# Kernel optimization log

Measured on AMD Instinct MI355X. Metric: run time of the kernel, lower is better.

Reference implementation:

```python
import jax, jax.numpy as jnp
import numpy as np

N = 100000   # nodes
B = 64       # graphs in batch
E = 1600000  # edges
D_IN = 2
W1D = W2D = W3D = 128
N_CLASSES = 3
MIN_SCORE = 0.1
TOL = 1e-7
BN_EPS = 1e-5


def setup_inputs() -> dict:
    key = jax.random.key(0)
    ks = jax.random.split(key, 32)
    inp = {}
    inp['x'] = jax.random.normal(ks[0], (N, D_IN), jnp.float32)
    inp['edge_index'] = jax.random.randint(ks[1], (2, E), 0, N, dtype=jnp.int32)
    inp['batch_index'] = jnp.sort(jax.random.randint(ks[2], (N,), 0, B, dtype=jnp.int32))
    inp['topk_w'] = jax.random.normal(ks[3], (D_IN,), jnp.float32)
    dims = [(D_IN, W1D), (W1D, W2D), (W2D, W3D)]
    k = 4
    for i, (din, dout) in enumerate(dims, start=1):
        inp[f'W{i}'] = jax.random.normal(ks[k], (din, dout), jnp.float32) * (1.0 / np.sqrt(din)); k += 1
        inp[f'b{i}'] = jax.random.normal(ks[k], (dout,), jnp.float32) * 0.05; k += 1
        inp[f'g{i}'] = 1.0 + 0.1 * jax.random.normal(ks[k], (dout,), jnp.float32); k += 1
        inp[f'be{i}'] = 0.1 * jax.random.normal(ks[k], (dout,), jnp.float32); k += 1
        inp[f'rm{i}'] = 0.1 * jax.random.normal(ks[k], (dout,), jnp.float32); k += 1
        inp[f'rv{i}'] = 1.0 + 0.1 * jax.random.uniform(ks[k], (dout,), jnp.float32); k += 1
    inp['linW'] = jax.random.normal(ks[k], (W3D, N_CLASSES), jnp.float32) * (1.0 / np.sqrt(W3D)); k += 1
    inp['linb'] = jax.random.normal(ks[k], (N_CLASSES,), jnp.float32) * 0.05
    return inp


def _bn_eval(x, g, be, rm, rv):
    # BatchNorm1d in eval mode (running stats)
    return (x - rm) * jax.lax.rsqrt(rv + BN_EPS) * g + be


def _gcn(x, src, dst, ew, W, b):
    # GCNConv: lin -> symmetric-normalized scatter-add (self-loops already in src/dst/ew)
    xw = x @ W                                   # [N, dout]
    deg = jax.ops.segment_sum(ew, dst, num_segments=N)
    dinv = jnp.where(deg > 0, jax.lax.rsqrt(deg), 0.0)
    norm = dinv[src] * ew * dinv[dst]            # [E+N]
    out = jax.ops.segment_sum(norm[:, None] * xw[src], dst, num_segments=N)
    return out + b


def reference(x, edge_index, batch_index, topk_w,
              W1, b1, g1, be1, rm1, rv1,
              W2, b2, g2, be2, rm2, rv2,
              W3, b3, g3, be3, rm3, rv3,
              linW, linb):
    # ---- TopKPooling (min_score mode): per-graph softmax score, threshold keep,
    # x scaled by score. Implemented via masking (fixed shapes): dropped nodes get
    # zero features, zero edge weights, and -inf at the max pool -> math identical
    # to PyG's node filtering (BN is eval-mode, i.e. per-node).
    logits = x @ topk_w                                                    # [N]
    m = jax.ops.segment_max(logits, batch_index, num_segments=B)
    e = jnp.exp(logits - m[batch_index])
    score = e / jax.ops.segment_sum(e, batch_index, num_segments=B)[batch_index]
    smax = jax.ops.segment_max(score, batch_index, num_segments=B)[batch_index] - TOL
    keep = score > jnp.minimum(smax, MIN_SCORE)                            # [N] bool
    keep_f = keep.astype(x.dtype)
    h = x * (score * keep_f)[:, None]

    src0, dst0 = edge_index[0], edge_index[1]
    loop = jnp.arange(N, dtype=src0.dtype)
    src = jnp.concatenate([src0, loop])
    dst = jnp.concatenate([dst0, loop])
    ew = jnp.concatenate([keep_f[src0] * keep_f[dst0], keep_f])            # mask + self-loops

    h = _bn_eval(jax.nn.relu(_gcn(h, src, dst, ew, W1, b1)), g1, be1, rm1, rv1)
    h = _bn_eval(jax.nn.relu(_gcn(h, src, dst, ew, W2, b2)), g2, be2, rm2, rv2)
    h = _bn_eval(jax.nn.relu(_gcn(h, src, dst, ew, W3, b3)), g3, be3, rm3, rv3)

    neg = jnp.finfo(h.dtype).min
    h = jnp.where(keep[:, None], h, neg)
    pooled = jax.ops.segment_max(h, batch_index, num_segments=B)           # [B, w3]
    out = pooled @ linW + linb
    return jax.nn.log_softmax(out, axis=1)
```

## Files before the change

### kernel.cpp

```cpp
#include <hip/hip_runtime.h>

#define NN 100000
#define BB 64
#define EE 1600000
#define FD 128
#define SLOTC 64
#define KSLOTS (BB * SLOTC)
#define EMAXE (1 << 20)
#define NWORDS (NN / 32)
#define STR 391

__device__ __forceinline__ int plower(const int* __restrict__ bidx, int v,
                                      int tid, int* ired) {
    int p = tid * STR;
    int val = bidx[p];
    ired[tid] = (val < v) ? tid : -1;
    __syncthreads();
    for (int s = 128; s > 0; s >>= 1) { if (tid < s) ired[tid] = max(ired[tid], ired[tid + s]); __syncthreads(); }
    int t0 = ired[0];
    __syncthreads();
    if (t0 < 0) return 0;
    int lo = t0 * STR;
    int hi = lo + STR; if (hi > NN) hi = NN;
    int ans = hi;
    for (int q = lo + 1 + tid; q < hi; q += 256) {
        if (bidx[q] >= v) { ans = q; break; }
    }
    ired[tid] = ans;
    __syncthreads();
    for (int s = 128; s > 0; s >>= 1) { if (tid < s) ired[tid] = min(ired[tid], ired[tid + s]); __syncthreads(); }
    int r = ired[0];
    __syncthreads();
    return r;
}

__global__ __launch_bounds__(256) void k_scorekeep(
    const float2* __restrict__ x, const int* __restrict__ bidx,
    const float* __restrict__ tw,
    unsigned* __restrict__ kfbits, int* __restrict__ nslot,
    int* __restrict__ knt, float* __restrict__ degs, float2* __restrict__ h0s,
    int* __restrict__ kecnt)
{
    __shared__ int   ired[256];
    __shared__ float red[256];
    __shared__ int   klist[SLOTC];
    __shared__ int   lcnt;
    __shared__ float shv;
    int b = blockIdx.x, tid = threadIdx.x;
    if (tid == 0) { lcnt = 0; if (b == 0) { kecnt[0] = 0; kecnt[1] = 0; } }
    int s0 = plower(bidx, b, tid, ired);
    int e0 = plower(bidx, b + 1, tid, ired);
    int L = e0 - s0;
    float w0 = tw[0], w1 = tw[1];

    if (L > 0) {
        int wlo = s0 >> 5, whi = (e0 - 1) >> 5;
        for (int w = wlo + tid; w <= whi; w += 256) {
            unsigned mask = 0xFFFFFFFFu;
            if (w == wlo) mask &= (0xFFFFFFFFu << (s0 & 31));
            if (w == whi) mask &= (0xFFFFFFFFu >> (31 - ((e0 - 1) & 31)));
            if (mask == 0xFFFFFFFFu) kfbits[w] = 0u;
            else atomicAnd(&kfbits[w], ~mask);
        }
    }

    float mx = -3.4028235e38f;
    for (int j = tid; j < L; j += 256) {
        float2 v = x[s0 + j];
        mx = fmaxf(mx, v.x * w0 + v.y * w1);
    }
    red[tid] = mx; __syncthreads();
    for (int s = 128; s > 0; s >>= 1) { if (tid < s) red[tid] = fmaxf(red[tid], red[tid + s]); __syncthreads(); }
    if (tid == 0) shv = red[0];
    __syncthreads();
    float m = shv;

    float sm = 0.f;
    for (int j = tid; j < L; j += 256) {
        float2 v = x[s0 + j];
        sm += expf(v.x * w0 + v.y * w1 - m);
    }
    red[tid] = sm; __syncthreads();
    for (int s = 128; s > 0; s >>= 1) { if (tid < s) red[tid] += red[tid + s]; __syncthreads(); }
    if (tid == 0) shv = red[0];
    __syncthreads();
    float S = shv;
    float thr = fminf(1.0f / S - 1e-7f, 0.1f);

    for (int j = tid; j < L; j += 256) {
        float2 v = x[s0 + j];
        float sc = expf(v.x * w0 + v.y * w1 - m) / S;
        if (sc > thr) {
            int l = atomicAdd(&lcnt, 1);
            if (l < SLOTC) klist[l] = j;
        }
    }
    __syncthreads();
    int nk = lcnt; if (nk > SLOTC) nk = SLOTC;
    if (tid == 0) knt[b] = nk;
    for (int l = tid; l < nk; l += 256) {
        int i = s0 + klist[l];
        float2 v = x[i];
        float sc = expf(v.x * w0 + v.y * w1 - m) / S;
        int slot = b * SLOTC + l;
        atomicOr(&kfbits[i >> 5], 1u << (i & 31));
        nslot[i] = slot;
        degs[slot] = 1.0f;
        h0s[slot] = make_float2(v.x * sc, v.y * sc);
    }
}

__global__ void k_edges(const int4* __restrict__ src4, const int* __restrict__ ei,
                        const unsigned* __restrict__ kfbits, const int* __restrict__ nslot,
                        float* __restrict__ degs, int* __restrict__ kedge,
                        int* __restrict__ kecnt) {
    int t = blockIdx.x * 256 + threadIdx.x;
    if (t * 4 >= EE) return;
    int4 s4 = src4[t];
    int ss[4] = {s4.x, s4.y, s4.z, s4.w};
    #pragma unroll
    for (int q = 0; q < 4; q++) {
        int s = ss[q];
        if ((kfbits[s >> 5] >> (s & 31)) & 1u) {
            int d = ei[EE + t * 4 + q];
            if ((kfbits[d >> 5] >> (d & 31)) & 1u) {
                int ds = nslot[d], sl = nslot[s];
                atomicAdd(&degs[ds], 1.0f);
                int idx = atomicAdd(&kecnt[0], 1);
                if (idx < EMAXE) { kedge[2 * idx] = sl; kedge[2 * idx + 1] = ds; }
                if ((sl >> 6) != (ds >> 6)) atomicAdd(&kecnt[1], 1);
            }
        }
    }
}

__global__ __launch_bounds__(256) void k_tail_main(
    const float* __restrict__ degs, const float2* __restrict__ h0s,
    const int* __restrict__ kedge, const int* __restrict__ kecnt,
    const int* __restrict__ knt,
    const float* __restrict__ W1, const float* __restrict__ b1,
    const float* __restrict__ g1, const float* __restrict__ be1,
    const float* __restrict__ rm1, const float* __restrict__ rv1,
    const float* __restrict__ W2, const float* __restrict__ b2,
    const float* __restrict__ g2, const float* __restrict__ be2,
    const float* __restrict__ rm2, const float* __restrict__ rv2,
    const float* __restrict__ W3, const float* __restrict__ b3,
    const float* __restrict__ g3, const float* __restrict__ be3,
    const float* __restrict__ rm3, const float* __restrict__ rv3,
    const float* __restrict__ linW, const float* __restrict__ linb,
    float* __restrict__ hY, float* __restrict__ out)
{
    __shared__ float tileA[SLOTC * FD];
    __shared__ float tileB[SLOTC * FD];
    __shared__ float2 psl[SLOTC];
    __shared__ float poolv[FD];
    __shared__ int keS;
    int b = blockIdx.x, tid = threadIdx.x;
    if (tid == 0) { int k = kecnt[0]; keS = k > EMAXE ? EMAXE : k; }
    for (int j = tid; j < SLOTC; j += 256) psl[j] = make_float2(0.f, 0.f);
    __syncthreads();
    int ke = keS, nk = knt[b], cross = kecnt[1];

    for (int t = tid; t < ke; t += 256) {
        int d = kedge[2 * t + 1];
        if ((d >> 6) == b) {
            int s = kedge[2 * t];
            float nm = rsqrtf(degs[s]) * rsqrtf(degs[d]);
            float2 h = h0s[s];
            atomicAdd(&psl[d & 63].x, nm * h.x);
            atomicAdd(&psl[d & 63].y, nm * h.y);
        }
    }
    __syncthreads();
    for (int j = tid; j < nk * FD; j += 256) {
        int ld = j >> 7, f = j & 127, slot = b * SLOTC + ld;
        float di = rsqrtf(degs[slot]), d2 = di * di;
        float2 h = h0s[slot];
        float a0 = psl[ld].x + d2 * h.x;
        float a1 = psl[ld].y + d2 * h.y;
        float v = a0 * W1[f] + a1 * W1[FD + f] + b1[f];
        v = fmaxf(v, 0.f);
        v = (v - rm1[f]) * rsqrtf(rv1[f] + 1e-5f) * g1[f] + be1[f];
        tileA[j] = v;
    }
    __syncthreads();
    for (int j = tid; j < nk * FD; j += 256) {
        int ld = j >> 7, f = j & 127;
        const float* xr = tileA + ld * FD;
        float acc = 0.f;
        #pragma unroll 8
        for (int k = 0; k < FD; k++) acc += xr[k] * W2[k * FD + f];
        tileB[j] = acc;
    }
    __syncthreads();
    if (cross != 0) {
        for (int j = tid; j < nk * FD; j += 256) {
            int ld = j >> 7, f = j & 127;
            hY[(b * SLOTC + ld) * FD + f] = tileB[j];
        }
        return;
    }
    for (int j = tid; j < nk * FD; j += 256) tileA[j] = 0.f;
    __syncthreads();
    for (long long idx = tid; idx < (long long)ke * FD; idx += 256) {
        int e = (int)(idx >> 7), f = (int)(idx & 127);
        int d = kedge[2 * e + 1];
        if ((d >> 6) == b) {
            int s = kedge[2 * e];
            float nm = rsqrtf(degs[s]) * rsqrtf(degs[d]);
            atomicAdd(&tileA[(d & 63) * FD + f], nm * tileB[(s & 63) * FD + f]);
        }
    }
    __syncthreads();
    for (int j = tid; j < nk * FD; j += 256) {
        int ld = j >> 7, f = j & 127, slot = b * SLOTC + ld;
        float di = rsqrtf(degs[slot]);
        float v = tileA[j] + di * di * tileB[j] + b2[f];
        v = fmaxf(v, 0.f);
        v = (v - rm2[f]) * rsqrtf(rv2[f] + 1e-5f) * g2[f] + be2[f];
        tileA[j] = v;
    }
    __syncthreads();
    for (int j = tid; j < nk * FD; j += 256) {
        int ld = j >> 7, f = j & 127;
        const float* xr = tileA + ld * FD;
        float acc = 0.f;
        #pragma unroll 8
        for (int k = 0; k < FD; k++) acc += xr[k] * W3[k * FD + f];
        tileB[j] = acc;
    }
    __syncthreads();
    for (int j = tid; j < nk * FD; j += 256) tileA[j] = 0.f;
    __syncthreads();
    for (long long idx = tid; idx < (long long)ke * FD; idx += 256) {
        int e = (int)(idx >> 7), f = (int)(idx & 127);
        int d = kedge[2 * e + 1];
        if ((d >> 6) == b) {
            int s = kedge[2 * e];
            float nm = rsqrtf(degs[s]) * rsqrtf(degs[d]);
            atomicAdd(&tileA[(d & 63) * FD + f], nm * tileB[(s & 63) * FD + f]);
        }
    }
    __syncthreads();
    for (int j = tid; j < nk * FD; j += 256) {
        int ld = j >> 7, f = j & 127, slot = b * SLOTC + ld;
        float di = rsqrtf(degs[slot]);
        float v = tileA[j] + di * di * tileB[j] + b3[f];
        v = fmaxf(v, 0.f);
        v = (v - rm3[f]) * rsqrtf(rv3[f] + 1e-5f) * g3[f] + be3[f];
        tileA[j] = v;
    }
    __syncthreads();
    for (int f = tid; f < FD; f += 256) {
        float mx = -3.4028235e38f;
        for (int ld = 0; ld < nk; ld++) mx = fmaxf(mx, tileA[ld * FD + f]);
        poolv[f] = mx;
    }
    __syncthreads();
    if (tid == 0) {
        float z0 = linb[0], z1 = linb[1], z2 = linb[2];
        for (int f = 0; f < FD; f++) {
            float pv = poolv[f];
            z0 += pv * linW[f * 3 + 0];
            z1 += pv * linW[f * 3 + 1];
            z2 += pv * linW[f * 3 + 2];
        }
        float m = fmaxf(z0, fmaxf(z1, z2));
        float l = m + logf(expf(z0 - m) + expf(z1 - m) + expf(z2 - m));
        out[b * 3 + 0] = z0 - l;
        out[b * 3 + 1] = z1 - l;
        out[b * 3 + 2] = z2 - l;
    }
}

__global__ __launch_bounds__(256) void k_tail_slow(
    const float* __restrict__ degs, const int* __restrict__ kedge,
    const int* __restrict__ kecnt, const int* __restrict__ knt,
    const float* __restrict__ hY,
    const float* __restrict__ b2, const float* __restrict__ g2,
    const float* __restrict__ be2, const float* __restrict__ rm2,
    const float* __restrict__ rv2,
    const float* __restrict__ W3, const float* __restrict__ b3,
    const float* __restrict__ g3, const float* __restrict__ be3,
    const float* __restrict__ rm3, const float* __restrict__ rv3,
    const float* __restrict__ linW, const float* __restrict__ linb,
    float* __restrict__ out)
{
    if (kecnt[1] == 0) return;
    __shared__ float tileA[SLOTC * FD];
    __shared__ float tileB[SLOTC * FD];
    __shared__ float rowt[FD];
    __shared__ float poolv[FD];
    __shared__ int keS;
    int b = blockIdx.x, tid = threadIdx.x;
    if (tid == 0) { int k = kecnt[0]; keS = k > EMAXE ? EMAXE : k; }
    __syncthreads();
    int ke = keS, nk = knt[b];

    for (int j = tid; j < nk * FD; j += 256) tileA[j] = 0.f;
    __syncthreads();
    for (long long idx = tid; idx < (long long)ke * FD; idx += 256) {
        int e = (int)(idx >> 7), f = (int)(idx & 127);
        int d = kedge[2 * e + 1];
        if ((d >> 6) == b) {
            int s = kedge[2 * e];
            float nm = rsqrtf(degs[s]) * rsqrtf(degs[d]);
            atomicAdd(&tileA[(d & 63) * FD + f], nm * hY[s * FD + f]);
        }
    }
    __syncthreads();
    for (int j = tid; j < nk * FD; j += 256) {
        int ld = j >> 7, f = j & 127, slot = b * SLOTC + ld;
        float di = rsqrtf(degs[slot]);
        float v = tileA[j] + di * di * hY[slot * FD + f] + b2[f];
        v = fmaxf(v, 0.f);
        v = (v - rm2[f]) * rsqrtf(rv2[f] + 1e-5f) * g2[f] + be2[f];
        tileA[j] = v;
    }
    __syncthreads();
    for (int j = tid; j < nk * FD; j += 256) {
        int ld = j >> 7, f = j & 127;
        const float* xr = tileA + ld * FD;
        float acc = 0.f;
        #pragma unroll 8
        for (int k = 0; k < FD; k++) acc += xr[k] * W3[k * FD + f];
        tileB[j] = acc;
    }
    __syncthreads();
    for (int j = tid; j < nk * FD; j += 256) tileA[j] = 0.f;
    __syncthreads();
    for (long long idx = tid; idx < (long long)ke * FD; idx += 256) {
        int e = (int)(idx >> 7), f = (int)(idx & 127);
        int d = kedge[2 * e + 1];
        if ((d >> 6) == b) {
            int s = kedge[2 * e];
            if ((s >> 6) == b) {
                float nm = rsqrtf(degs[s]) * rsqrtf(degs[d]);
                atomicAdd(&tileA[(d & 63) * FD + f], nm * tileB[(s & 63) * FD + f]);
            }
        }
    }
    __syncthreads();
    for (int e = 0; e < ke; e++) {
        int d = kedge[2 * e + 1];
        if ((d >> 6) != b) continue;
        int s = kedge[2 * e];
        if ((s >> 6) == b) continue;
        float dis = rsqrtf(degs[s]);
        for (int f = tid; f < FD; f += 256) {
            float acc = dis * dis * hY[s * FD + f];
            for (int e2 = 0; e2 < ke; e2++) {
                if (kedge[2 * e2 + 1] == s) {
                    int u = kedge[2 * e2];
                    acc += rsqrtf(degs[u]) * dis * hY[u * FD + f];
                }
            }
            float v = acc + b2[f];
            v = fmaxf(v, 0.f);
            v = (v - rm2[f]) * rsqrtf(rv2[f] + 1e-5f) * g2[f] + be2[f];
            rowt[f] = v;
        }
        __syncthreads();
        float nm = dis * rsqrtf(degs[d]);
        for (int f = tid; f < FD; f += 256) {
            float acc = 0.f;
            #pragma unroll 8
            for (int k = 0; k < FD; k++) acc += rowt[k] * W3[k * FD + f];
            atomicAdd(&tileA[(d & 63) * FD + f], nm * acc);
        }
        __syncthreads();
    }
    for (int j = tid; j < nk * FD; j += 256) {
        int ld = j >> 7, f = j & 127, slot = b * SLOTC + ld;
        float di = rsqrtf(degs[slot]);
        float v = tileA[j] + di * di * tileB[j] + b3[f];
        v = fmaxf(v, 0.f);
        v = (v - rm3[f]) * rsqrtf(rv3[f] + 1e-5f) * g3[f] + be3[f];
        tileA[j] = v;
    }
    __syncthreads();
    for (int f = tid; f < FD; f += 256) {
        float mx = -3.4028235e38f;
        for (int ld = 0; ld < nk; ld++) mx = fmaxf(mx, tileA[ld * FD + f]);
        poolv[f] = mx;
    }
    __syncthreads();
    if (tid == 0) {
        float z0 = linb[0], z1 = linb[1], z2 = linb[2];
        for (int f = 0; f < FD; f++) {
            float pv = poolv[f];
            z0 += pv * linW[f * 3 + 0];
            z1 += pv * linW[f * 3 + 1];
            z2 += pv * linW[f * 3 + 2];
        }
        float m = fmaxf(z0, fmaxf(z1, z2));
        float l = m + logf(expf(z0 - m) + expf(z1 - m) + expf(z2 - m));
        out[b * 3 + 0] = z0 - l;
        out[b * 3 + 1] = z1 - l;
        out[b * 3 + 2] = z2 - l;
    }
}

extern "C" void kernel_launch(void* const* d_in, const int* in_sizes, int n_in,
                              void* d_out, int out_size, void* d_ws, size_t ws_size,
                              hipStream_t stream) {
    (void)in_sizes; (void)n_in; (void)out_size; (void)ws_size;
    const float* x    = (const float*)d_in[0];
    const int*   ei   = (const int*)d_in[1];
    const int*   bidx = (const int*)d_in[2];
    const float* tw   = (const float*)d_in[3];
    const float* W1 = (const float*)d_in[4],  *b1 = (const float*)d_in[5],  *g1 = (const float*)d_in[6];
    const float* be1= (const float*)d_in[7],  *rm1= (const float*)d_in[8],  *rv1= (const float*)d_in[9];
    const float* W2 = (const float*)d_in[10], *b2 = (const float*)d_in[11], *g2 = (const float*)d_in[12];
    const float* be2= (const float*)d_in[13], *rm2= (const float*)d_in[14], *rv2= (const float*)d_in[15];
    const float* W3 = (const float*)d_in[16], *b3 = (const float*)d_in[17], *g3 = (const float*)d_in[18];
    const float* be3= (const float*)d_in[19], *rm3= (const float*)d_in[20], *rv3= (const float*)d_in[21];
    const float* linW = (const float*)d_in[22], *linb = (const float*)d_in[23];
    float* out = (float*)d_out;

    char* w = (char*)d_ws;
    auto take = [&](size_t bytes) { char* r = w; w += (bytes + 255) & ~(size_t)255; return r; };
    int*      kecnt  = (int*)take(16);
    int*      knt    = (int*)take((size_t)BB * 4);
    unsigned* kfbits = (unsigned*)take((size_t)NWORDS * 4);
    int*      nslot  = (int*)take((size_t)NN * 4);
    float*    degs   = (float*)take((size_t)KSLOTS * 4);
    float2*   h0s    = (float2*)take((size_t)KSLOTS * 8);
    int*      kedge  = (int*)take((size_t)EMAXE * 8);
    float*    hY     = (float*)take((size_t)KSLOTS * FD * 4);

    k_scorekeep<<<BB, 256, 0, stream>>>((const float2*)x, bidx, tw,
                                        kfbits, nslot, knt, degs, h0s, kecnt);
    k_edges<<<(EE / 4 + 255) / 256, 256, 0, stream>>>((const int4*)ei, ei, kfbits,
                                                      nslot, degs, kedge, kecnt);
    k_tail_main<<<BB, 256, 0, stream>>>(degs, h0s, kedge, kecnt, knt,
                                        W1, b1, g1, be1, rm1, rv1,
                                        W2, b2, g2, be2, rm2, rv2,
                                        W3, b3, g3, be3, rm3, rv3,
                                        linW, linb, hY, out);
    k_tail_slow<<<BB, 256, 0, stream>>>(degs, kedge, kecnt, knt, hY,
                                        b2, g2, be2, rm2, rv2,
                                        W3, b3, g3, be3, rm3, rv3,
                                        linW, linb, out);
}
```

Baseline: 143.2 us.

## Fuse score, edge filter and GCN tail into one cooperative kernel

Merges the four kernel launches into a single cooperative kernel of 256 blocks that uses grid-wide syncs between the scoring, edge-filtering and tail phases. The edge phase becomes a grid-stride loop over all edges. The aim is to remove per-launch overhead and inter-kernel gaps, and it keeps the old multi-kernel path as a fallback if the cooperative launch fails. In exchange, the edge scan runs on far fewer blocks than the previous 1563, the shared-memory footprint per block grows because score and tail storage are combined, and grid syncs add their own cost.

```diff
diff --git a/kernel.cpp b/kernel.cpp
--- a/kernel.cpp
+++ b/kernel.cpp
@@ -1,4 +1,7 @@
 #include <hip/hip_runtime.h>
+#include <hip/hip_cooperative_groups.h>
+
+namespace cg = cooperative_groups;
 
 #define NN 100000
 #define BB 64
@@ -9,6 +12,21 @@
 #define EMAXE (1 << 20)
 #define NWORDS (NN / 32)
 #define STR 391
+#define GRID_F 256
+
+struct KArgs {
+    const float2* x; const int4* src4; const int* ei; const int* bidx; const float* tw;
+    const float *W1,*b1,*g1,*be1,*rm1,*rv1;
+    const float *W2,*b2,*g2,*be2,*rm2,*rv2;
+    const float *W3,*b3,*g3,*be3,*rm3,*rv3;
+    const float *linW,*linb;
+    unsigned* kfbits; int* nslot; int* knt; float* degs; float2* h0s;
+    int* kedge; int* kecnt; float* hY; float* out;
+};
+
+struct LdsScore { int ired[256]; float red[256]; int klist[SLOTC]; int lcnt; float shv; };
+struct LdsTail  { float tileA[SLOTC*FD]; float tileB[SLOTC*FD]; float2 psl[SLOTC];
+                  float poolv[FD]; float rowt[FD]; };
 
 __device__ __forceinline__ int plower(const int* __restrict__ bidx, int v,
                                       int tid, int* ired) {
@@ -34,371 +52,356 @@
     return r;
 }
 
-__global__ __launch_bounds__(256) void k_scorekeep(
-    const float2* __restrict__ x, const int* __restrict__ bidx,
-    const float* __restrict__ tw,
-    unsigned* __restrict__ kfbits, int* __restrict__ nslot,
-    int* __restrict__ knt, float* __restrict__ degs, float2* __restrict__ h0s,
-    int* __restrict__ kecnt)
-{
-    __shared__ int   ired[256];
-    __shared__ float red[256];
-    __shared__ int   klist[SLOTC];
-    __shared__ int   lcnt;
-    __shared__ float shv;
-    int b = blockIdx.x, tid = threadIdx.x;
-    if (tid == 0) { lcnt = 0; if (b == 0) { kecnt[0] = 0; kecnt[1] = 0; } }
-    int s0 = plower(bidx, b, tid, ired);
-    int e0 = plower(bidx, b + 1, tid, ired);
-    int L = e0 - s0;
-    float w0 = tw[0], w1 = tw[1];
-
-    if (L > 0) {
+__device__ void phase_score(const KArgs& a, int b, int tid, LdsScore& L) {
+    if (tid == 0) { L.lcnt = 0; if (b == 0) { a.kecnt[0] = 0; a.kecnt[1] = 0; } }
+    int s0 = plower(a.bidx, b, tid, L.ired);
+    int e0 = plower(a.bidx, b + 1, tid, L.ired);
+    int Ln = e0 - s0;
+    float w0 = a.tw[0], w1 = a.tw[1];
+
+    if (Ln > 0) {
         int wlo = s0 >> 5, whi = (e0 - 1) >> 5;
         for (int w = wlo + tid; w <= whi; w += 256) {
             unsigned mask = 0xFFFFFFFFu;
             if (w == wlo) mask &= (0xFFFFFFFFu << (s0 & 31));
             if (w == whi) mask &= (0xFFFFFFFFu >> (31 - ((e0 - 1) & 31)));
-            if (mask == 0xFFFFFFFFu) kfbits[w] = 0u;
-            else atomicAnd(&kfbits[w], ~mask);
+            if (mask == 0xFFFFFFFFu) a.kfbits[w] = 0u;
+            else atomicAnd(&a.kfbits[w], ~mask);
         }
     }
 
     float mx = -3.4028235e38f;
-    for (int j = tid; j < L; j += 256) {
-        float2 v = x[s0 + j];
+    for (int j = tid; j < Ln; j += 256) {
+        float2 v = a.x[s0 + j];
         mx = fmaxf(mx, v.x * w0 + v.y * w1);
     }
-    red[tid] = mx; __syncthreads();
-    for (int s = 128; s > 0; s >>= 1) { if (tid < s) red[tid] = fmaxf(red[tid], red[tid + s]); __syncthreads(); }
-    if (tid == 0) shv = red[0];
-    __syncthreads();
-    float m = shv;
+    L.red[tid] = mx; __syncthreads();
+    for (int s = 128; s > 0; s >>= 1) { if (tid < s) L.red[tid] = fmaxf(L.red[tid], L.red[tid + s]); __syncthreads(); }
+    if (tid == 0) L.shv = L.red[0];
+    __syncthreads();
+    float m = L.shv;
 
     float sm = 0.f;
-    for (int j = tid; j < L; j += 256) {
-        float2 v = x[s0 + j];
+    for (int j = tid; j < Ln; j += 256) {
+        float2 v = a.x[s0 + j];
         sm += expf(v.x * w0 + v.y * w1 - m);
     }
-    red[tid] = sm; __syncthreads();
-    for (int s = 128; s > 0; s >>= 1) { if (tid < s) red[tid] += red[tid + s]; __syncthreads(); }
-    if (tid == 0) shv = red[0];
-    __syncthreads();
-    float S = shv;
+    L.red[tid] = sm; __syncthreads();
+    for (int s = 128; s > 0; s >>= 1) { if (tid < s) L.red[tid] += L.red[tid + s]; __syncthreads(); }
+    if (tid == 0) L.shv = L.red[0];
+    __syncthreads();
+    float S = L.shv;
     float thr = fminf(1.0f / S - 1e-7f, 0.1f);
 
-    for (int j = tid; j < L; j += 256) {
-        float2 v = x[s0 + j];
+    for (int j = tid; j < Ln; j += 256) {
+        float2 v = a.x[s0 + j];
         float sc = expf(v.x * w0 + v.y * w1 - m) / S;
         if (sc > thr) {
-            int l = atomicAdd(&lcnt, 1);
-            if (l < SLOTC) klist[l] = j;
-        }
-    }
-    __syncthreads();
-    int nk = lcnt; if (nk > SLOTC) nk = SLOTC;
-    if (tid == 0) knt[b] = nk;
+            int l = atomicAdd(&L.lcnt, 1);
+            if (l < SLOTC) L.klist[l] = j;
+        }
+    }
+    __syncthreads();
+    int nk = L.lcnt; if (nk > SLOTC) nk = SLOTC;
+    if (tid == 0) a.knt[b] = nk;
     for (int l = tid; l < nk; l += 256) {
-        int i = s0 + klist[l];
-        float2 v = x[i];
+        int i = s0 + L.klist[l];
+        float2 v = a.x[i];
         float sc = expf(v.x * w0 + v.y * w1 - m) / S;
         int slot = b * SLOTC + l;
-        atomicOr(&kfbits[i >> 5], 1u << (i & 31));
-        nslot[i] = slot;
-        degs[slot] = 1.0f;
-        h0s[slot] = make_float2(v.x * sc, v.y * sc);
-    }
-}
-
-__global__ void k_edges(const int4* __restrict__ src4, const int* __restrict__ ei,
-                        const unsigned* __restrict__ kfbits, const int* __restrict__ nslot,
-                        float* __restrict__ degs, int* __restrict__ kedge,
-                        int* __restrict__ kecnt) {
-    int t = blockIdx.x * 256 + threadIdx.x;
-    if (t * 4 >= EE) return;
-    int4 s4 = src4[t];
-    int ss[4] = {s4.x, s4.y, s4.z, s4.w};
-    #pragma unroll
-    for (int q = 0; q < 4; q++) {
-        int s = ss[q];
-        if ((kfbits[s >> 5] >> (s & 31)) & 1u) {
-            int d = ei[EE + t * 4 + q];
-            if ((kfbits[d >> 5] >> (d & 31)) & 1u) {
-                int ds = nslot[d], sl = nslot[s];
-                atomicAdd(&degs[ds], 1.0f);
-                int idx = atomicAdd(&kecnt[0], 1);
-                if (idx < EMAXE) { kedge[2 * idx] = sl; kedge[2 * idx + 1] = ds; }
-                if ((sl >> 6) != (ds >> 6)) atomicAdd(&kecnt[1], 1);
+        atomicOr(&a.kfbits[i >> 5], 1u << (i & 31));
+        a.nslot[i] = slot;
+        a.degs[slot] = 1.0f;
+        a.h0s[slot] = make_float2(v.x * sc, v.y * sc);
+    }
+}
+
+__device__ void phase_edges(const KArgs& a, int t0, int stride) {
+    const int M = EE / 4;
+    for (int t = t0; t < M; t += stride) {
+        int4 s4 = a.src4[t];
+        int ss[4] = {s4.x, s4.y, s4.z, s4.w};
+        #pragma unroll
+        for (int q = 0; q < 4; q++) {
+            int s = ss[q];
+            if ((a.kfbits[s >> 5] >> (s & 31)) & 1u) {
+                int d = a.ei[EE + t * 4 + q];
+                if ((a.kfbits[d >> 5] >> (d & 31)) & 1u) {
+                    int ds = a.nslot[d], sl = a.nslot[s];
+                    atomicAdd(&a.degs[ds], 1.0f);
+                    int idx = atomicAdd(&a.kecnt[0], 1);
+                    if (idx < EMAXE) { a.kedge[2 * idx] = sl; a.kedge[2 * idx + 1] = ds; }
+                    if ((sl >> 6) != (ds >> 6)) atomicAdd(&a.kecnt[1], 1);
+                }
             }
         }
     }
 }
 
-__global__ __launch_bounds__(256) void k_tail_main(
-    const float* __restrict__ degs, const float2* __restrict__ h0s,
-    const int* __restrict__ kedge, const int* __restrict__ kecnt,
-    const int* __restrict__ knt,
-    const float* __restrict__ W1, const float* __restrict__ b1,
-    const float* __restrict__ g1, const float* __restrict__ be1,
-    const float* __restrict__ rm1, const float* __restrict__ rv1,
-    const float* __restrict__ W2, const float* __restrict__ b2,
-    const float* __restrict__ g2, const float* __restrict__ be2,
-    const float* __restrict__ rm2, const float* __restrict__ rv2,
-    const float* __restrict__ W3, const float* __restrict__ b3,
-    const float* __restrict__ g3, const float* __restrict__ be3,
-    const float* __restrict__ rm3, const float* __restrict__ rv3,
-    const float* __restrict__ linW, const float* __restrict__ linb,
-    float* __restrict__ hY, float* __restrict__ out)
-{
-    __shared__ float tileA[SLOTC * FD];
-    __shared__ float tileB[SLOTC * FD];
-    __shared__ float2 psl[SLOTC];
-    __shared__ float poolv[FD];
-    __shared__ int keS;
-    int b = blockIdx.x, tid = threadIdx.x;
-    if (tid == 0) { int k = kecnt[0]; keS = k > EMAXE ? EMAXE : k; }
-    for (int j = tid; j < SLOTC; j += 256) psl[j] = make_float2(0.f, 0.f);
-    __syncthreads();
-    int ke = keS, nk = knt[b], cross = kecnt[1];
-
+__device__ void tail_common(const KArgs& a, int b, int tid, LdsTail& T, int ke, int nk) {
+    for (int j = tid; j < SLOTC; j += 256) T.psl[j] = make_float2(0.f, 0.f);
+    __syncthreads();
     for (int t = tid; t < ke; t += 256) {
-        int d = kedge[2 * t + 1];
+        int d = a.kedge[2 * t + 1];
         if ((d >> 6) == b) {
-            int s = kedge[2 * t];
-            float nm = rsqrtf(degs[s]) * rsqrtf(degs[d]);
-            float2 h = h0s[s];
-            atomicAdd(&psl[d & 63].x, nm * h.x);
-            atomicAdd(&psl[d & 63].y, nm * h.y);
+            int s = a.kedge[2 * t];
+            float nm = rsqrtf(a.degs[s]) * rsqrtf(a.degs[d]);
+            float2 h = a.h0s[s];
+            atomicAdd(&T.psl[d & 63].x, nm * h.x);
+            atomicAdd(&T.psl[d & 63].y, nm * h.y);
         }
     }
     __syncthreads();
     for (int j = tid; j < nk * FD; j += 256) {
         int ld = j >> 7, f = j & 127, slot = b * SLOTC + ld;
-        float di = rsqrtf(degs[slot]), d2 = di * di;
-        float2 h = h0s[slot];
-        float a0 = psl[ld].x + d2 * h.x;
-        float a1 = psl[ld].y + d2 * h.y;
-        float v = a0 * W1[f] + a1 * W1[FD + f] + b1[f];
+        float di = rsqrtf(a.degs[slot]), d2 = di * di;
+        float2 h = a.h0s[slot];
+        float a0 = T.psl[ld].x + d2 * h.x;
+        float a1 = T.psl[ld].y + d2 * h.y;
+        float v = a0 * a.W1[f] + a1 * a.W1[FD + f] + a.b1[f];
         v = fmaxf(v, 0.f);
-        v = (v - rm1[f]) * rsqrtf(rv1[f] + 1e-5f) * g1[f] + be1[f];
-        tileA[j] = v;
+        v = (v - a.rm1[f]) * rsqrtf(a.rv1[f] + 1e-5f) * a.g1[f] + a.be1[f];
+        T.tileA[j] = v;
     }
     __syncthreads();
     for (int j = tid; j < nk * FD; j += 256) {
         int ld = j >> 7, f = j & 127;
-        const float* xr = tileA + ld * FD;
+        const float* xr = T.tileA + ld * FD;
         float acc = 0.f;
         #pragma unroll 8
-        for (int k = 0; k < FD; k++) acc += xr[k] * W2[k * FD + f];
-        tileB[j] = acc;
-    }
-    __syncthreads();
-    if (cross != 0) {
-        for (int j = tid; j < nk * FD; j += 256) {
-            int ld = j >> 7, f = j & 127;
-            hY[(b * SLOTC + ld) * FD + f] = tileB[j];
-        }
-        return;
-    }
-    for (int j = tid; j < nk * FD; j += 256) tileA[j] = 0.f;
+        for (int k = 0; k < FD; k++) acc += xr[k] * a.W2[k * FD + f];
+        T.tileB[j] = acc;
+    }
+    __syncthreads();
+}
+
+__device__ void tail_write_hY(const KArgs& a, int b, int tid, LdsTail& T, int nk) {
+    for (int j = tid; j < nk * FD; j += 256) {
+        int ld = j >> 7, f = j & 127;
+        a.hY[(b * SLOTC + ld) * FD + f] = T.tileB[j];
+    }
+}
+
+__device__ void tail_out(const KArgs& a, int b, int tid, LdsTail& T, int nk) {
+    for (int f = tid; f < FD; f += 256) {
+        float mx = -3.4028235e38f;
+        for (int ld = 0; ld < nk; ld++) mx = fmaxf(mx, T.tileA[ld * FD + f]);
+        T.poolv[f] = mx;
+    }
+    __syncthreads();
+    if (tid == 0) {
+        float z0 = a.linb[0], z1 = a.linb[1], z2 = a.linb[2];
+        for (int f = 0; f < FD; f++) {
+            float pv = T.poolv[f];
+            z0 += pv * a.linW[f * 3 + 0];
+            z1 += pv * a.linW[f * 3 + 1];
+            z2 += pv * a.linW[f * 3 + 2];
+        }
+        float m = fmaxf(z0, fmaxf(z1, z2));
+        float l = m + logf(expf(z0 - m) + expf(z1 - m) + expf(z2 - m));
+        a.out[b * 3 + 0] = z0 - l;
+        a.out[b * 3 + 1] = z1 - l;
+        a.out[b * 3 + 2] = z2 - l;
+    }
+}
+
+__device__ void tail_fast(const KArgs& a, int b, int tid, LdsTail& T, int ke, int nk) {
+    for (int j = tid; j < nk * FD; j += 256) T.tileA[j] = 0.f;
     __syncthreads();
     for (long long idx = tid; idx < (long long)ke * FD; idx += 256) {
         int e = (int)(idx >> 7), f = (int)(idx & 127);
-        int d = kedge[2 * e + 1];
+        int d = a.kedge[2 * e + 1];
         if ((d >> 6) == b) {
-            int s = kedge[2 * e];
-            float nm = rsqrtf(degs[s]) * rsqrtf(degs[d]);
-            atomicAdd(&tileA[(d & 63) * FD + f], nm * tileB[(s & 63) * FD + f]);
+            int s = a.kedge[2 * e];
+            float nm = rsqrtf(a.degs[s]) * rsqrtf(a.degs[d]);
+            atomicAdd(&T.tileA[(d & 63) * FD + f], nm * T.tileB[(s & 63) * FD + f]);
         }
     }
     __syncthreads();
     for (int j = tid; j < nk * FD; j += 256) {
         int ld = j >> 7, f = j & 127, slot = b * SLOTC + ld;
-        float di = rsqrtf(degs[slot]);
-        float v = tileA[j] + di * di * tileB[j] + b2[f];
+        float di = rsqrtf(a.degs[slot]);
+        float v = T.tileA[j] + di * di * T.tileB[j] + a.b2[f];
         v = fmaxf(v, 0.f);
-        v = (v - rm2[f]) * rsqrtf(rv2[f] + 1e-5f) * g2[f] + be2[f];
-        tileA[j] = v;
+        v = (v - a.rm2[f]) * rsqrtf(a.rv2[f] + 1e-5f) * a.g2[f] + a.be2[f];
+        T.tileA[j] = v;
     }
     __syncthreads();
     for (int j = tid; j < nk * FD; j += 256) {
         int ld = j >> 7, f = j & 127;
-        const float* xr = tileA + ld * FD;
+        const float* xr = T.tileA + ld * FD;
         float acc = 0.f;
         #pragma unroll 8
-        for (int k = 0; k < FD; k++) acc += xr[k] * W3[k * FD + f];
-        tileB[j] = acc;
-    }
-    __syncthreads();
-    for (int j = tid; j < nk * FD; j += 256) tileA[j] = 0.f;
+        for (int k = 0; k < FD; k++) acc += xr[k] * a.W3[k * FD + f];
+        T.tileB[j] = acc;
+    }
+    __syncthreads();
+    for (int j = tid; j < nk * FD; j += 256) T.tileA[j] = 0.f;
     __syncthreads();
     for (long long idx = tid; idx < (long long)ke * FD; idx += 256) {
         int e = (int)(idx >> 7), f = (int)(idx & 127);
-        int d = kedge[2 * e + 1];
+        int d = a.kedge[2 * e + 1];
         if ((d >> 6) == b) {
-            int s = kedge[2 * e];
-            float nm = rsqrtf(degs[s]) * rsqrtf(degs[d]);
-            atomicAdd(&tileA[(d & 63) * FD + f], nm * tileB[(s & 63) * FD + f]);
+            int s = a.kedge[2 * e];
+            float nm = rsqrtf(a.degs[s]) * rsqrtf(a.degs[d]);
+            atomicAdd(&T.tileA[(d & 63) * FD + f], nm * T.tileB[(s & 63) * FD + f]);
         }
     }
     __syncthreads();
     for (int j = tid; j < nk * FD; j += 256) {
         int ld = j >> 7, f = j & 127, slot = b * SLOTC + ld;
-        float di = rsqrtf(degs[slot]);
-        float v = tileA[j] + di * di * tileB[j] + b3[f];
+        float di = rsqrtf(a.degs[slot]);
+        float v = T.tileA[j] + di * di * T.tileB[j] + a.b3[f];
         v = fmaxf(v, 0.f);
-        v = (v - rm3[f]) * rsqrtf(rv3[f] + 1e-5f) * g3[f] + be3[f];
-        tileA[j] = v;
-    }
-    __syncthreads();
-    for (int f = tid; f < FD; f += 256) {
-        float mx = -3.4028235e38f;
-        for (int ld = 0; ld < nk; ld++) mx = fmaxf(mx, tileA[ld * FD + f]);
-        poolv[f] = mx;
-    }
-    __syncthreads();
-    if (tid == 0) {
-        float z0 = linb[0], z1 = linb[1], z2 = linb[2];
-        for (int f = 0; f < FD; f++) {
-            float pv = poolv[f];
-            z0 += pv * linW[f * 3 + 0];
-            z1 += pv * linW[f * 3 + 1];
-            z2 += pv * linW[f * 3 + 2];
-        }
-        float m = fmaxf(z0, fmaxf(z1, z2));
-        float l = m + logf(expf(z0 - m) + expf(z1 - m) + expf(z2 - m));
-        out[b * 3 + 0] = z0 - l;
-        out[b * 3 + 1] = z1 - l;
-        out[b * 3 + 2] = z2 - l;
-    }
-}
-
-__global__ __launch_bounds__(256) void k_tail_slow(
-    const float* __restrict__ degs, const int* __restrict__ kedge,
-    const int* __restrict__ kecnt, const int* __restrict__ knt,
-    const float* __restrict__ hY,
-    const float* __restrict__ b2, const float* __restrict__ g2,
-    const float* __restrict__ be2, const float* __restrict__ rm2,
-    const float* __restrict__ rv2,
-    const float* __restrict__ W3, const float* __restrict__ b3,
-    const float* __restrict__ g3, const float* __restrict__ be3,
-    const float* __restrict__ rm3, const float* __restrict__ rv3,
-    const float* __restrict__ linW, const float* __restrict__ linb,
-    float* __restrict__ out)
-{
-    if (kecnt[1] == 0) return;
-    __shared__ float tileA[SLOTC * FD];
-    __shared__ float tileB[SLOTC * FD];
-    __shared__ float rowt[FD];
-    __shared__ float poolv[FD];
-    __shared__ int keS;
-    int b = blockIdx.x, tid = threadIdx.x;
-    if (tid == 0) { int k = kecnt[0]; keS = k > EMAXE ? EMAXE : k; }
-    __syncthreads();
-    int ke = keS, nk = knt[b];
-
-    for (int j = tid; j < nk * FD; j += 256) tileA[j] = 0.f;
+        v = (v - a.rm3[f]) * rsqrtf(a.rv3[f] + 1e-5f) * a.g3[f] + a.be3[f];
+        T.tileA[j] = v;
+    }
+    __syncthreads();
+    tail_out(a, b, tid, T, nk);
+}
+
+__device__ void tail_slow(const KArgs& a, int b, int tid, LdsTail& T, int ke, int nk) {
+    for (int j = tid; j < nk * FD; j += 256) T.tileA[j] = 0.f;
     __syncthreads();
     for (long long idx = tid; idx < (long long)ke * FD; idx += 256) {
         int e = (int)(idx >> 7), f = (int)(idx & 127);
-        int d = kedge[2 * e + 1];
+        int d = a.kedge[2 * e + 1];
         if ((d >> 6) == b) {
-            int s = kedge[2 * e];
-            float nm = rsqrtf(degs[s]) * rsqrtf(degs[d]);
-            atomicAdd(&tileA[(d & 63) * FD + f], nm * hY[s * FD + f]);
+            int s = a.kedge[2 * e];
+            float nm = rsqrtf(a.degs[s]) * rsqrtf(a.degs[d]);
+            atomicAdd(&T.tileA[(d & 63) * FD + f], nm * a.hY[s * FD + f]);
         }
     }
     __syncthreads();
     for (int j = tid; j < nk * FD; j += 256) {
         int ld = j >> 7, f = j & 127, slot = b * SLOTC + ld;
-        float di = rsqrtf(degs[slot]);
-        float v = tileA[j] + di * di * hY[slot * FD + f] + b2[f];
+        float di = rsqrtf(a.degs[slot]);
+        float v = T.tileA[j] + di * di * a.hY[slot * FD + f] + a.b2[f];
         v = fmaxf(v, 0.f);
-        v = (v - rm2[f]) * rsqrtf(rv2[f] + 1e-5f) * g2[f] + be2[f];
-        tileA[j] = v;
+        v = (v - a.rm2[f]) * rsqrtf(a.rv2[f] + 1e-5f) * a.g2[f] + a.be2[f];
+        T.tileA[j] = v;
     }
     __syncthreads();
     for (int j = tid; j < nk * FD; j += 256) {
         int ld = j >> 7, f = j & 127;
-        const float* xr = tileA + ld * FD;
+        const float* xr = T.tileA + ld * FD;
         float acc = 0.f;
         #pragma unroll 8
-        for (int k = 0; k < FD; k++) acc += xr[k] * W3[k * FD + f];
-        tileB[j] = acc;
-    }
-    __syncthreads();
-    for (int j = tid; j < nk * FD; j += 256) tileA[j] = 0.f;
+        for (int k = 0; k < FD; k++) acc += xr[k] * a.W3[k * FD + f];
+        T.tileB[j] = acc;
+    }
+    __syncthreads();
+    for (int j = tid; j < nk * FD; j += 256) T.tileA[j] = 0.f;
     __syncthreads();
     for (long long idx = tid; idx < (long long)ke * FD; idx += 256) {
         int e = (int)(idx >> 7), f = (int)(idx & 127);
-        int d = kedge[2 * e + 1];
+        int d = a.kedge[2 * e + 1];
         if ((d >> 6) == b) {
-            int s = kedge[2 * e];
+            int s = a.kedge[2 * e];
             if ((s >> 6) == b) {
-                float nm = rsqrtf(degs[s]) * rsqrtf(degs[d]);
-                atomicAdd(&tileA[(d & 63) * FD + f], nm * tileB[(s & 63) * FD + f]);
+                float nm = rsqrtf(a.degs[s]) * rsqrtf(a.degs[d]);
+                atomicAdd(&T.tileA[(d & 63) * FD + f], nm * T.tileB[(s & 63) * FD + f]);
             }
         }
     }
     __syncthreads();
     for (int e = 0; e < ke; e++) {
-        int d = kedge[2 * e + 1];
+        int d = a.kedge[2 * e + 1];
         if ((d >> 6) != b) continue;
-        int s = kedge[2 * e];
+        int s = a.kedge[2 * e];
         if ((s >> 6) == b) continue;
-        float dis = rsqrtf(degs[s]);
+        float dis = rsqrtf(a.degs[s]);
         for (int f = tid; f < FD; f += 256) {
-            float acc = dis * dis * hY[s * FD + f];
+            float acc = dis * dis * a.hY[s * FD + f];
             for (int e2 = 0; e2 < ke; e2++) {
-                if (kedge[2 * e2 + 1] == s) {
-                    int u = kedge[2 * e2];
-                    acc += rsqrtf(degs[u]) * dis * hY[u * FD + f];
+                if (a.kedge[2 * e2 + 1] == s) {
+                    int u = a.kedge[2 * e2];
+                    acc += rsqrtf(a.degs[u]) * dis * a.hY[u * FD + f];
                 }
             }
-            float v = acc + b2[f];
+            float v = acc + a.b2[f];
             v = fmaxf(v, 0.f);
-            v = (v - rm2[f]) * rsqrtf(rv2[f] + 1e-5f) * g2[f] + be2[f];
-            rowt[f] = v;
+            v = (v - a.rm2[f]) * rsqrtf(a.rv2[f] + 1e-5f) * a.g2[f] + a.be2[f];
+            T.rowt[f] = v;
         }
         __syncthreads();
-        float nm = dis * rsqrtf(degs[d]);
+        float nm = dis * rsqrtf(a.degs[d]);
         for (int f = tid; f < FD; f += 256) {
             float acc = 0.f;
             #pragma unroll 8
-            for (int k = 0; k < FD; k++) acc += rowt[k] * W3[k * FD + f];
-            atomicAdd(&tileA[(d & 63) * FD + f], nm * acc);
+            for (int k = 0; k < FD; k++) acc += T.rowt[k] * a.W3[k * FD + f];
+            atomicAdd(&T.tileA[(d & 63) * FD + f], nm * acc);
         }
         __syncthreads();
     }
     for (int j = tid; j < nk * FD; j += 256) {
         int ld = j >> 7, f = j & 127, slot = b * SLOTC + ld;
-        float di = rsqrtf(degs[slot]);
-        float v = tileA[j] + di * di * tileB[j] + b3[f];
+        float di = rsqrtf(a.degs[slot]);
+        float v = T.tileA[j] + di * di * T.tileB[j] + a.b3[f];
         v = fmaxf(v, 0.f);
-        v = (v - rm3[f]) * rsqrtf(rv3[f] + 1e-5f) * g3[f] + be3[f];
-        tileA[j] = v;
-    }
-    __syncthreads();
-    for (int f = tid; f < FD; f += 256) {
-        float mx = -3.4028235e38f;
-        for (int ld = 0; ld < nk; ld++) mx = fmaxf(mx, tileA[ld * FD + f]);
-        poolv[f] = mx;
-    }
-    __syncthreads();
-    if (tid == 0) {
-        float z0 = linb[0], z1 = linb[1], z2 = linb[2];
-        for (int f = 0; f < FD; f++) {
-            float pv = poolv[f];
-            z0 += pv * linW[f * 3 + 0];
-            z1 += pv * linW[f * 3 + 1];
-            z2 += pv * linW[f * 3 + 2];
-        }
-        float m = fmaxf(z0, fmaxf(z1, z2));
-        float l = m + logf(expf(z0 - m) + expf(z1 - m) + expf(z2 - m));
-        out[b * 3 + 0] = z0 - l;
-        out[b * 3 + 1] = z1 - l;
-        out[b * 3 + 2] = z2 - l;
-    }
+        v = (v - a.rm3[f]) * rsqrtf(a.rv3[f] + 1e-5f) * a.g3[f] + a.be3[f];
+        T.tileA[j] = v;
+    }
+    __syncthreads();
+    tail_out(a, b, tid, T, nk);
+}
+
+__global__ __launch_bounds__(256) void k_fused(KArgs a) {
+    __shared__ LdsScore L;
+    __shared__ LdsTail T;
+    cg::grid_group g = cg::this_grid();
+    int blk = blockIdx.x, tid = threadIdx.x;
+
+    if (blk < BB) phase_score(a, blk, tid, L);
+    g.sync();
+    phase_edges(a, blk * 256 + tid, GRID_F * 256);
+    g.sync();
+
+    int ke = a.kecnt[0]; if (ke > EMAXE) ke = EMAXE;
+    int cross = a.kecnt[1];
+    if (blk < BB) {
+        int nk = a.knt[blk];
+        tail_common(a, blk, tid, T, ke, nk);
+        if (cross == 0) tail_fast(a, blk, tid, T, ke, nk);
+        else            tail_write_hY(a, blk, tid, T, nk);
+    }
+    if (cross != 0) {
+        g.sync();
+        if (blk < BB) {
+            int nk = a.knt[blk];
+            tail_slow(a, blk, tid, T, ke, nk);
+        }
+    }
+}
+
+__global__ __launch_bounds__(256) void k_scorekeep(KArgs a) {
+    __shared__ LdsScore L;
+    phase_score(a, blockIdx.x, threadIdx.x, L);
+}
+
+__global__ void k_edges(KArgs a) {
+    int t = blockIdx.x * 256 + threadIdx.x;
+    phase_edges(a, t, 1 << 30);
+}
+
+__global__ __launch_bounds__(256) void k_tail_main(KArgs a) {
+    __shared__ LdsTail T;
+    int b = blockIdx.x, tid = threadIdx.x;
+    int ke = a.kecnt[0]; if (ke > EMAXE) ke = EMAXE;
+    int cross = a.kecnt[1];
+    int nk = a.knt[b];
+    tail_common(a, b, tid, T, ke, nk);
+    if (cross != 0) { tail_write_hY(a, b, tid, T, nk); return; }
+    tail_fast(a, b, tid, T, ke, nk);
+}
+
+__global__ __launch_bounds__(256) void k_tail_slow(KArgs a) {
+    if (a.kecnt[1] == 0) return;
+    __shared__ LdsTail T;
+    int b = blockIdx.x, tid = threadIdx.x;
+    int ke = a.kecnt[0]; if (ke > EMAXE) ke = EMAXE;
+    int nk = a.knt[b];
+    tail_slow(a, b, tid, T, ke, nk);
 }
 
 extern "C" void kernel_launch(void* const* d_in, const int* in_sizes, int n_in,
@@ -409,14 +412,6 @@
     const int*   ei   = (const int*)d_in[1];
     const int*   bidx = (const int*)d_in[2];
     const float* tw   = (const float*)d_in[3];
-    const float* W1 = (const float*)d_in[4],  *b1 = (const float*)d_in[5],  *g1 = (const float*)d_in[6];
-    const float* be1= (const float*)d_in[7],  *rm1= (const float*)d_in[8],  *rv1= (const float*)d_in[9];
-    const float* W2 = (const float*)d_in[10], *b2 = (const float*)d_in[11], *g2 = (const float*)d_in[12];
-    const float* be2= (const float*)d_in[13], *rm2= (const float*)d_in[14], *rv2= (const float*)d_in[15];
-    const float* W3 = (const float*)d_in[16], *b3 = (const float*)d_in[17], *g3 = (const float*)d_in[18];
-    const float* be3= (const float*)d_in[19], *rm3= (const float*)d_in[20], *rv3= (const float*)d_in[21];
-    const float* linW = (const float*)d_in[22], *linb = (const float*)d_in[23];
-    float* out = (float*)d_out;
 
     char* w = (char*)d_ws;
     auto take = [&](size_t bytes) { char* r = w; w += (bytes + 255) & ~(size_t)255; return r; };
@@ -429,17 +424,25 @@
     int*      kedge  = (int*)take((size_t)EMAXE * 8);
     float*    hY     = (float*)take((size_t)KSLOTS * FD * 4);
 
-    k_scorekeep<<<BB, 256, 0, stream>>>((const float2*)x, bidx, tw,
-                                        kfbits, nslot, knt, degs, h0s, kecnt);
-    k_edges<<<(EE / 4 + 255) / 256, 256, 0, stream>>>((const int4*)ei, ei, kfbits,
-                                                      nslot, degs, kedge, kecnt);
-    k_tail_main<<<BB, 256, 0, stream>>>(degs, h0s, kedge, kecnt, knt,
-                                        W1, b1, g1, be1, rm1, rv1,
-                                        W2, b2, g2, be2, rm2, rv2,
-                                        W3, b3, g3, be3, rm3, rv3,
-                                        linW, linb, hY, out);
-    k_tail_slow<<<BB, 256, 0, stream>>>(degs, kedge, kecnt, knt, hY,
-                                        b2, g2, be2, rm2, rv2,
-                                        W3, b3, g3, be3, rm3, rv3,
-                                        linW, linb, out);
-}
+    KArgs ka;
+    ka.x = (const float2*)x; ka.src4 = (const int4*)ei; ka.ei = ei; ka.bidx = bidx; ka.tw = tw;
+    ka.W1 = (const float*)d_in[4];  ka.b1 = (const float*)d_in[5];  ka.g1 = (const float*)d_in[6];
+    ka.be1= (const float*)d_in[7];  ka.rm1= (const float*)d_in[8];  ka.rv1= (const float*)d_in[9];
+    ka.W2 = (const float*)d_in[10]; ka.b2 = (const float*)d_in[11]; ka.g2 = (const float*)d_in[12];
+    ka.be2= (const float*)d_in[13]; ka.rm2= (const float*)d_in[14]; ka.rv2= (const float*)d_in[15];
+    ka.W3 = (const float*)d_in[16]; ka.b3 = (const float*)d_in[17]; ka.g3 = (const float*)d_in[18];
+    ka.be3= (const float*)d_in[19]; ka.rm3= (const float*)d_in[20]; ka.rv3= (const float*)d_in[21];
+    ka.linW = (const float*)d_in[22]; ka.linb = (const float*)d_in[23];
+    ka.kfbits = kfbits; ka.nslot = nslot; ka.knt = knt; ka.degs = degs; ka.h0s = h0s;
+    ka.kedge = kedge; ka.kecnt = kecnt; ka.hY = hY; ka.out = (float*)d_out;
+
+    void* params[] = { (void*)&ka };
+    hipError_t err = hipLaunchCooperativeKernel(reinterpret_cast<const void*>(k_fused),
+                                                dim3(GRID_F), dim3(256), params, 0, stream);
+    if (err != hipSuccess) {
+        hipLaunchKernelGGL(k_scorekeep, dim3(BB), dim3(256), 0, stream, ka);
+        hipLaunchKernelGGL(k_edges, dim3((EE / 4 + 255) / 256), dim3(256), 0, stream, ka);
+        hipLaunchKernelGGL(k_tail_main, dim3(BB), dim3(256), 0, stream, ka);
+        hipLaunchKernelGGL(k_tail_slow, dim3(BB), dim3(256), 0, stream, ka);
+    }
+}
```

Result: slower. 255.1 us (+78.1%).
